# Kernel tuning notes

Hardware: AMD Instinct MI355X
Metric: run time of the kernel (lower is better)

Reference implementation:

```python
import math
import jax, jax.numpy as jnp
import numpy as np

HID = 2048      # hidden_size
NH = 16         # num_heads
KD = HID // NH  # key head dim = 128 (even, required by XPOS)
VD = HID        # value_dim (value_factor=1)
VHD = VD // NH  # value head dim
SCALE_BASE = 512
ROPE_BASE = 10000.0
GN_EPS = 1e-5


def _rotate_every_two(x):
    x1 = x[..., ::2]
    x2 = x[..., 1::2]
    return jnp.stack((-x2, x1), axis=-1).reshape(x.shape)


def _dup(a):  # repeat_interleave(x, 2, dim=-1)
    return jnp.repeat(a, 2, axis=-1)


def _xpos_apply(x, pos, inv_freq, xpos_scale, downscale):
    # x: [B, H, S, KD], pos: [B, S]
    posf = pos.astype(jnp.float32)
    angles = posf[:, :, None] * inv_freq[None, None, :]          # [B, S, KD/2]
    sin = _dup(jnp.sin(angles))[:, None]                          # [B, 1, S, KD]
    cos = _dup(jnp.cos(angles))[:, None]
    scale = xpos_scale[None, None, :] ** (posf[:, :, None] / SCALE_BASE)
    if downscale:
        scale = 1.0 / scale
    scale = _dup(scale)[:, None]                                  # [B, 1, S, KD]
    return (x * cos + _rotate_every_two(x) * sin) * scale


def setup_inputs() -> dict:
    key = jax.random.key(0)
    ks = jax.random.split(key, 6)
    B, S = 1, 2048
    std = 1.0 / HID
    x = jax.random.normal(ks[0], (B, S, HID), dtype=jnp.float32)
    position_ids = jnp.broadcast_to(jnp.arange(S, dtype=jnp.int64), (B, S))
    Wq = jax.random.normal(ks[1], (HID, HID), dtype=jnp.float32) * std
    Wk = jax.random.normal(ks[2], (HID, HID), dtype=jnp.float32) * std
    Wv = jax.random.normal(ks[3], (HID, VD), dtype=jnp.float32) * std
    Wg = jax.random.normal(ks[4], (HID, VD), dtype=jnp.float32) * std
    Wo = jax.random.normal(ks[5], (VD, HID), dtype=jnp.float32) * std
    gn_weight = jnp.ones((VD,), dtype=jnp.float32)
    gn_bias = jnp.zeros((VD,), dtype=jnp.float32)
    return {"x": x, "position_ids": position_ids, "Wq": Wq, "Wk": Wk,
            "Wv": Wv, "Wg": Wg, "Wo": Wo,
            "gn_weight": gn_weight, "gn_bias": gn_bias}


def reference(x, position_ids, Wq, Wk, Wv, Wg, Wo, gn_weight, gn_bias):
    B, S, _ = x.shape
    # XPOS / multiscale-decay buffers (deterministic, as in XPOSRelativePosition)
    inv_freq = 1.0 / (ROPE_BASE ** (jnp.arange(0, KD, 2, dtype=jnp.float32) / KD))
    xpos_scale = (jnp.arange(0, KD, 2, dtype=jnp.float32) + 0.4 * KD) / (1.4 * KD)
    gamma = 1.0 - jnp.exp(jnp.linspace(math.log(1.0 / 32), math.log(1.0 / 512), NH))
    log_gamma = jnp.log(gamma)                                    # [NH]

    # projections -> [B, H, S, d]
    q = (x @ Wq).reshape(B, S, NH, KD).transpose(0, 2, 1, 3)
    k = (x @ Wk).reshape(B, S, NH, KD).transpose(0, 2, 1, 3)
    v = (x @ Wv).reshape(B, S, NH, VHD).transpose(0, 2, 1, 3)
    g = x @ Wg                                                    # [B, S, VD]

    q = _xpos_apply(q, position_ids, inv_freq, xpos_scale, downscale=False)
    k = _xpos_apply(k, position_ids, inv_freq, xpos_scale, downscale=True)

    # decay mask: exp(log_gamma * (i-j)) for i>=j else 0   [B, H, S, S]
    relpos = position_ids[:, :, None] - position_ids[:, None, :]  # [B, S, S]
    decay = jnp.exp(log_gamma[None, :, None, None]
                    * jnp.maximum(relpos, 0)[:, None].astype(jnp.float32))
    decay = decay * (relpos >= 0)[:, None].astype(jnp.float32)

    scores = jnp.einsum('bhqd,bhkd->bhqk', q, k) * decay          # [B, H, S, S]
    retained = jnp.einsum('bhqk,bhkv->bhqv', scores, v)           # [B, H, S, VHD]

    # GroupNorm(num_heads, value_dim): normalize each head group per token
    r = retained.transpose(0, 2, 1, 3)                            # [B, S, H, VHD]
    mean = r.mean(axis=-1, keepdims=True)
    var = r.var(axis=-1, keepdims=True)
    rn = (r - mean) * jax.lax.rsqrt(var + GN_EPS)
    rn = rn * gn_weight.reshape(NH, VHD) + gn_bias.reshape(NH, VHD)
    rn = rn.reshape(B, S, VD)

    out = (jax.nn.silu(g) * rn) @ Wo                              # [B, S, HID]
    return out
```

## Files before the change

kernel.cpp:

```cpp
#include <hip/hip_runtime.h>
#include <math.h>

#define S_LEN 2048
#define HIDD  2048
#define NHEAD 16
#define HD    128

#define TILE_SH 4096

typedef __attribute__((ext_vector_type(8))) short short8;
typedef __attribute__((ext_vector_type(4))) float float4v;
typedef unsigned short ushort_t;

static __device__ __forceinline__ ushort_t f2bf(float f) {
    unsigned int u = __float_as_uint(f);
    u += 0x7fff + ((u >> 16) & 1);
    return (ushort_t)(u >> 16);
}
static __device__ __forceinline__ float bf2f(ushort_t s) {
    return __uint_as_float(((unsigned int)s) << 16);
}
__device__ __forceinline__ float silu_f(float x) { return x / (1.f + expf(-x)); }

__device__ __forceinline__ void gl_lds16(const ushort_t* g, short* l) {
    __builtin_amdgcn_global_load_lds((const __attribute__((address_space(1))) void*)g,
                                     (__attribute__((address_space(3))) void*)l, 16, 0, 0);
}

__global__ __launch_bounds__(256)
void split_kernel(const float* __restrict__ in, ushort_t* __restrict__ hi,
                  ushort_t* __restrict__ lo, int n4)
{
    const int i = blockIdx.x * 256 + threadIdx.x;
    if (i >= n4) return;
    const float4 v = ((const float4*)in)[i];
    ushort4 h, l;
    h.x = f2bf(v.x); l.x = f2bf(v.x - bf2f(h.x));
    h.y = f2bf(v.y); l.y = f2bf(v.y - bf2f(h.y));
    h.z = f2bf(v.z); l.z = f2bf(v.z - bf2f(h.z));
    h.w = f2bf(v.w); l.w = f2bf(v.w - bf2f(h.w));
    const int row = i >> 9, c4 = (i & 511) * 4;
    const size_t off = ((size_t)((row >> 7) * 64 + (c4 >> 5))) * TILE_SH
                     + (row & 127) * 32 + (c4 & 31);
    *(ushort4*)&hi[off] = h;
    *(ushort4*)&lo[off] = l;
}

__global__ __launch_bounds__(256)
void addp_kernel(float* __restrict__ out, const float* __restrict__ p, int n4)
{
    const int i = blockIdx.x * 256 + threadIdx.x;
    if (i >= n4) return;
    float4 a = ((const float4*)out)[i];
    const float4 b = ((const float4*)p)[i];
    a.x += b.x; a.y += b.y; a.z += b.z; a.w += b.w;
    ((float4*)out)[i] = a;
}

__global__ __launch_bounds__(256)
void split_transpose_all(const float* __restrict__ W0, const float* __restrict__ W1,
                         const float* __restrict__ W2, const float* __restrict__ W3,
                         const float* __restrict__ W4, ushort_t* __restrict__ wt)
{
    __shared__ float t[64][65];
    const size_t PL = (size_t)HIDD * HIDD;
    const int z = blockIdx.z;
    const float* W = (z == 0) ? W0 : (z == 1) ? W1 : (z == 2) ? W2 : (z == 3) ? W3 : W4;
    ushort_t* Thi = wt + (size_t)z * 2 * PL;
    ushort_t* Tlo = Thi + PL;

    const int k0 = blockIdx.y * 64, n0 = blockIdx.x * 64;
    const int tx = threadIdx.x & 15, ty = threadIdx.x >> 4;
    #pragma unroll
    for (int it = 0; it < 4; it++) {
        const int k = ty + it * 16;
        const float4 v = *(const float4*)&W[(size_t)(k0 + k) * HIDD + n0 + tx * 4];
        t[k][tx * 4 + 0] = v.x; t[k][tx * 4 + 1] = v.y;
        t[k][tx * 4 + 2] = v.z; t[k][tx * 4 + 3] = v.w;
    }
    __syncthreads();
    #pragma unroll
    for (int it = 0; it < 4; it++) {
        const int n = ty + it * 16;
        ushort4 h, l; float a;
        a = t[tx * 4 + 0][n]; h.x = f2bf(a); l.x = f2bf(a - bf2f(h.x));
        a = t[tx * 4 + 1][n]; h.y = f2bf(a); l.y = f2bf(a - bf2f(h.y));
        a = t[tx * 4 + 2][n]; h.z = f2bf(a); l.z = f2bf(a - bf2f(h.z));
        a = t[tx * 4 + 3][n]; h.w = f2bf(a); l.w = f2bf(a - bf2f(h.w));
        const int nn_ = n0 + n, kk_ = k0 + tx * 4;
        const size_t off = ((size_t)((nn_ >> 7) * 64 + (kk_ >> 5))) * TILE_SH
                         + (nn_ & 127) * 32 + (kk_ & 31);
        *(ushort4*)&Thi[off] = h;
        *(ushort4*)&Tlo[off] = l;
    }
}

template<int MODE>
__global__ __launch_bounds__(256, 2)
void mfma_gemm(const ushort_t* __restrict__ Ahi, const ushort_t* __restrict__ Alo,
               const ushort_t* __restrict__ WT, const int* __restrict__ pos_ids,
               ushort_t* __restrict__ qhi, ushort_t* __restrict__ qlo,
               ushort_t* __restrict__ khi, ushort_t* __restrict__ klo,
               ushort_t* __restrict__ vThi, ushort_t* __restrict__ vTlo,
               float* __restrict__ gbuf, float* __restrict__ outC, int mbase)
{
    __shared__ __align__(16) short sm[(MODE == 1) ? 16896 : 8448];

    const int tid = threadIdx.x;
    const int w = tid >> 6, L = tid & 63;
    const int qd = L >> 4, lc = L & 15;
    const int lin = blockIdx.x;
    int n0, m0, kh = 0;
    if (MODE == 0) {
        n0 = (((lin & 7) << 3) + ((lin >> 3) & 7)) << 7;
        m0 = mbase + ((lin >> 6) << 7);
    } else {
        n0 = (lin & 15) << 7;
        m0 = ((lin >> 4) & 15) << 7;
        kh = lin >> 8;
    }
    const size_t PL = (size_t)HIDD * HIDD;

    int sel, nn;
    const ushort_t *Bhi, *Blo;
    if (MODE == 0) {
        sel = n0 >> 11; nn = n0 & 2047;
        Bhi = WT + (size_t)sel * 2 * PL; Blo = Bhi + PL;
    } else {
        sel = -1; nn = n0;
        Bhi = WT; Blo = WT + PL;
    }

    const int sdoff = (w >> 1) * 4096 + (w & 1) * 2048 + L * 8;
    const ushort_t* sbase = ((w < 2) ? Bhi : Blo) + (size_t)(nn >> 7) * 64 * TILE_SH
                          + (w & 1) * 2048 + L * 8;

    const ushort_t* aTh = Ahi + (size_t)(m0 >> 7) * 64 * TILE_SH;
    const ushort_t* aTl = Alo + (size_t)(m0 >> 7) * 64 * TILE_SH;

    const int wm = (w & 1) * 64, wn = (w >> 1) * 64;
    int aoff[4], boff[4];
    #pragma unroll
    for (int i = 0; i < 4; i++) aoff[i] = (wm + i * 16 + lc) * 32 + qd * 8;
    #pragma unroll
    for (int j = 0; j < 4; j++) boff[j] = (wn + j * 16 + lc) * 32 + qd * 8;

    float4v acc[4][4];
    #pragma unroll
    for (int i = 0; i < 4; i++)
        #pragma unroll
        for (int j = 0; j < 4; j++)
            #pragma unroll
            for (int r = 0; r < 4; r++) acc[i][j][r] = 0.f;

    const int kt0 = (MODE == 1) ? kh * 32 : 0;
    const int kt1 = (MODE == 1) ? kt0 + 32 : 64;

    if (MODE == 0) {
        for (int kt = kt0; kt < kt1; kt++) {
            const size_t ko = (size_t)kt * TILE_SH;
            short8 ahf[4], alf[4];
            #pragma unroll
            for (int i = 0; i < 4; i++) {
                ahf[i] = *(const short8*)(aTh + ko + aoff[i]);
                alf[i] = *(const short8*)(aTl + ko + aoff[i]);
            }
            #pragma unroll
            for (int t = 0; t < 4; t++)
                gl_lds16(sbase + ko + t * 512, sm + sdoff + t * 512);
            __syncthreads();

            short8 bhf[4], blf[4];
            #pragma unroll
            for (int j = 0; j < 4; j++) {
                bhf[j] = *(const short8*)(sm + boff[j]);
                blf[j] = *(const short8*)(sm + 4096 + boff[j]);
            }
            #pragma unroll
            for (int i = 0; i < 4; i++)
                #pragma unroll
                for (int j = 0; j < 4; j++) {
                    acc[i][j] = __builtin_amdgcn_mfma_f32_16x16x32_bf16(ahf[i], bhf[j], acc[i][j], 0, 0, 0);
                    acc[i][j] = __builtin_amdgcn_mfma_f32_16x16x32_bf16(alf[i], bhf[j], acc[i][j], 0, 0, 0);
                    acc[i][j] = __builtin_amdgcn_mfma_f32_16x16x32_bf16(ahf[i], blf[j], acc[i][j], 0, 0, 0);
                }
            __syncthreads();
        }
    } else {
        #pragma unroll
        for (int t = 0; t < 4; t++)
            gl_lds16(sbase + (size_t)kt0 * TILE_SH + t * 512, sm + sdoff + t * 512);
        asm volatile("s_waitcnt vmcnt(0)" ::: "memory");
        __builtin_amdgcn_s_barrier();
        __builtin_amdgcn_sched_barrier(0);

        int cur = 0;
        for (int kt = kt0; kt < kt1; kt++) {
            if (kt + 1 < kt1) {
                const size_t kn = (size_t)(kt + 1) * TILE_SH;
                short* nb = sm + (cur ^ 1) * 8192;
                #pragma unroll
                for (int t = 0; t < 4; t++)
                    gl_lds16(sbase + kn + t * 512, nb + sdoff + t * 512);
            }
            const size_t ko = (size_t)kt * TILE_SH;
            short8 ahf[4], alf[4];
            #pragma unroll
            for (int i = 0; i < 4; i++) {
                ahf[i] = *(const short8*)(aTh + ko + aoff[i]);
                alf[i] = *(const short8*)(aTl + ko + aoff[i]);
            }
            const short* cb = sm + cur * 8192;
            short8 bhf[4], blf[4];
            #pragma unroll
            for (int j = 0; j < 4; j++) {
                bhf[j] = *(const short8*)(cb + boff[j]);
                blf[j] = *(const short8*)(cb + 4096 + boff[j]);
            }
            #pragma unroll
            for (int i = 0; i < 4; i++)
                #pragma unroll
                for (int j = 0; j < 4; j++) {
                    acc[i][j] = __builtin_amdgcn_mfma_f32_16x16x32_bf16(ahf[i], bhf[j], acc[i][j], 0, 0, 0);
                    acc[i][j] = __builtin_amdgcn_mfma_f32_16x16x32_bf16(alf[i], bhf[j], acc[i][j], 0, 0, 0);
                    acc[i][j] = __builtin_amdgcn_mfma_f32_16x16x32_bf16(ahf[i], blf[j], acc[i][j], 0, 0, 0);
                }
            asm volatile("s_waitcnt vmcnt(0)" ::: "memory");
            __builtin_amdgcn_s_barrier();
            __builtin_amdgcn_sched_barrier(0);
            cur ^= 1;
        }
    }

    float* ob = (float*)sm;
    const int half = w & 1;
    const int head = nn >> 7;

    #pragma unroll
    for (int i = 0; i < 4; i++) {
        #pragma unroll
        for (int j = 0; j < 4; j++)
            #pragma unroll
            for (int r = 0; r < 4; r++)
                ob[(half * 16 + qd * 4 + r) * 132 + wn + j * 16 + lc] = acc[i][j][r];
        __syncthreads();

        if (MODE == 1 || sel == 3) {
            float* dst = (MODE == 1) ? (kh ? gbuf : outC) : gbuf;
            #pragma unroll
            for (int p = 0; p < 4; p++) {
                const int row = p * 8 + (tid >> 5);
                const int c = (tid & 31) * 4;
                const int grow = m0 + (row >> 4) * 64 + i * 16 + (row & 15);
                const float4 vv = *(const float4*)&ob[row * 132 + c];
                *(float4*)&dst[(size_t)grow * HIDD + nn + c] = vv;
            }
        } else if (sel == 2) {
            const int d = tid >> 1, hs = tid & 1;
            const int sbase2 = m0 + hs * 64 + i * 16;
            short8 h0, h1, l0, l1;
            #pragma unroll
            for (int sp = 0; sp < 8; sp++) {
                float a = ob[(hs * 16 + sp) * 132 + d];
                ushort_t hb = f2bf(a);
                h0[sp] = (short)hb; l0[sp] = (short)f2bf(a - bf2f(hb));
                a = ob[(hs * 16 + 8 + sp) * 132 + d];
                hb = f2bf(a);
                h1[sp] = (short)hb; l1[sp] = (short)f2bf(a - bf2f(hb));
            }
            ushort_t* dh = vThi + ((size_t)head * HD + d) * S_LEN + sbase2;
            ushort_t* dl = vTlo + ((size_t)head * HD + d) * S_LEN + sbase2;
            *(short8*)dh = h0; *(short8*)(dh + 8) = h1;
            *(short8*)dl = l0; *(short8*)(dl + 8) = l1;
        } else {
            const float sgn = (sel == 0) ? 1.f : -1.f;
            ushort_t* dhb = (sel == 0) ? qhi : khi;
            ushort_t* dlb = (sel == 0) ? qlo : klo;
            #pragma unroll
            for (int p = 0; p < 2; p++) {
                const int row = p * 16 + (tid >> 4);
                const int c8 = (tid & 15) * 8;
                const int grow = m0 + (row >> 4) * 64 + i * 16 + (row & 15);
                const float pos = (float)pos_ids[grow];
                const float pe = sgn * pos * (1.f / 512.f);
                short8 hv, lv;
                #pragma unroll
                for (int pp = 0; pp < 4; pp++) {
                    const int d = c8 + pp * 2;
                    const float v0 = ob[row * 132 + d], v1 = ob[row * 132 + d + 1];
                    const float invf = exp2f(-(float)d * (13.28771238f / 128.f));
                    float s, c_; sincosf(pos * invf, &s, &c_);
                    const float scl = exp2f(log2f(((float)d + 51.2f) * (1.f / 179.2f)) * pe);
                    const float e0 = (v0 * c_ - v1 * s) * scl;
                    const float e1 = (v1 * c_ + v0 * s) * scl;
                    const ushort_t h0 = f2bf(e0), h1 = f2bf(e1);
                    hv[pp * 2] = (short)h0;  hv[pp * 2 + 1] = (short)h1;
                    lv[pp * 2] = (short)f2bf(e0 - bf2f(h0));
                    lv[pp * 2 + 1] = (short)f2bf(e1 - bf2f(h1));
                }
                *(short8*)&dhb[((size_t)head * S_LEN + grow) * HD + c8] = hv;
                *(short8*)&dlb[((size_t)head * S_LEN + grow) * HD + c8] = lv;
            }
        }
        __syncthreads();
    }
}

#define KROW 136
#define VROW 40
#define KH_  0
#define KL_  (32 * KROW)
#define VH_  (2 * 32 * KROW)
#define VL_  (VH_ + 128 * VROW)
#define PH_  (VH_ + 2 * 128 * VROW)
#define PLO_ (PH_ + 64 * VROW)
#define YH_  8704
#define YL_  (YH_ + 64 * KROW)
__global__ __launch_bounds__(256, 2)
void retention2(const ushort_t* __restrict__ qhi, const ushort_t* __restrict__ qlo,
                const ushort_t* __restrict__ khi, const ushort_t* __restrict__ klo,
                const ushort_t* __restrict__ vThi, const ushort_t* __restrict__ vTlo,
                const float* __restrict__ gbuf, const float* __restrict__ gnw,
                const float* __restrict__ gnb,
                ushort_t* __restrict__ yhi, ushort_t* __restrict__ ylo)
{
    __shared__ __align__(16) short sm[26112];

    const int h = blockIdx.y;
    const int qb = (gridDim.x - 1) - blockIdx.x;
    const int r0 = qb * 64;
    const int tid = threadIdx.x;
    const int w = tid >> 6, L = tid & 63;
    const int qd = L >> 4, lc = L & 15;

    const float e = -3.4657359f + (float)h * ((-6.2383246f + 3.4657359f) / 15.f);
    const float lg2g = logf(1.f - expf(e)) * 1.44269504f;

    short8 qfh[4], qfl[4];
    {
        const size_t qb0 = ((size_t)h * S_LEN + r0 + w * 16 + lc) * HD + qd * 8;
        #pragma unroll
        for (int ks = 0; ks < 4; ks++) {
            qfh[ks] = *(const short8*)(qhi + qb0 + ks * 32);
            qfl[ks] = *(const short8*)(qlo + qb0 + ks * 32);
        }
    }

    float4v osum[2][4];
    #pragma unroll
    for (int mt = 0; mt < 2; mt++)
        #pragma unroll
        for (int j = 0; j < 4; j++)
            #pragma unroll
            for (int r = 0; r < 4; r++) osum[mt][j][r] = 0.f;

    const int qh_ = w >> 1, vh_ = w & 1;
    const int nch = (r0 + 64) / 32;

    for (int ch = 0; ch < nch; ch++) {
        const int kg0 = ch * 32;
        #pragma unroll
        for (int t = 0; t < 4; t++) {
            const int c = t * 256 + tid;
            const int p = c >> 9, r = (c >> 4) & 31, qq = c & 15;
            const ushort_t* src = (p ? klo : khi) + ((size_t)h * S_LEN + kg0 + r) * HD + qq * 8;
            *(short8*)(sm + (p ? KL_ : KH_) + r * KROW + qq * 8) = *(const short8*)src;
        }
        #pragma unroll
        for (int t = 0; t < 4; t++) {
            const int c = t * 256 + tid;
            const int p = c >> 9, r = (c >> 2) & 127, qq = c & 3;
            const ushort_t* src = (p ? vTlo : vThi) + ((size_t)h * HD + r) * S_LEN + kg0 + qq * 8;
            *(short8*)(sm + (p ? VL_ : VH_) + r * VROW + qq * 8) = *(const short8*)src;
        }
        __syncthreads();

        float4v sacc[2];
        #pragma unroll
        for (int j = 0; j < 2; j++)
            #pragma unroll
            for (int r = 0; r < 4; r++) sacc[j][r] = 0.f;
        #pragma unroll
        for (int ks = 0; ks < 4; ks++) {
            #pragma unroll
            for (int j = 0; j < 2; j++) {
                const short8 bh = *(const short8*)(sm + KH_ + (j * 16 + lc) * KROW + ks * 32 + qd * 8);
                const short8 bl = *(const short8*)(sm + KL_ + (j * 16 + lc) * KROW + ks * 32 + qd * 8);
                sacc[j] = __builtin_amdgcn_mfma_f32_16x16x32_bf16(qfh[ks], bh, sacc[j], 0, 0, 0);
                sacc[j] = __builtin_amdgcn_mfma_f32_16x16x32_bf16(qfl[ks], bh, sacc[j], 0, 0, 0);
                sacc[j] = __builtin_amdgcn_mfma_f32_16x16x32_bf16(qfh[ks], bl, sacc[j], 0, 0, 0);
            }
        }
        #pragma unroll
        for (int j = 0; j < 2; j++)
            #pragma unroll
            for (int r = 0; r < 4; r++) {
                const int dq = (r0 + w * 16 + qd * 4 + r) - (kg0 + j * 16 + lc);
                const float p = (dq >= 0) ? sacc[j][r] * exp2f(lg2g * (float)dq) : 0.f;
                const ushort_t hb = f2bf(p);
                const int off = (w * 16 + qd * 4 + r) * VROW + j * 16 + lc;
                sm[PH_ + off]  = (short)hb;
                sm[PLO_ + off] = (short)f2bf(p - bf2f(hb));
            }
        __syncthreads();

        #pragma unroll
        for (int mt = 0; mt < 2; mt++) {
            const short8 pfh = *(const short8*)(sm + PH_  + (qh_ * 32 + mt * 16 + lc) * VROW + qd * 8);
            const short8 pfl = *(const short8*)(sm + PLO_ + (qh_ * 32 + mt * 16 + lc) * VROW + qd * 8);
            #pragma unroll
            for (int j = 0; j < 4; j++) {
                const short8 vfh = *(const short8*)(sm + VH_ + (vh_ * 64 + j * 16 + lc) * VROW + qd * 8);
                const short8 vfl = *(const short8*)(sm + VL_ + (vh_ * 64 + j * 16 + lc) * VROW + qd * 8);
                osum[mt][j] = __builtin_amdgcn_mfma_f32_16x16x32_bf16(pfh, vfh, osum[mt][j], 0, 0, 0);
                osum[mt][j] = __builtin_amdgcn_mfma_f32_16x16x32_bf16(pfl, vfh, osum[mt][j], 0, 0, 0);
                osum[mt][j] = __builtin_amdgcn_mfma_f32_16x16x32_bf16(pfh, vfl, osum[mt][j], 0, 0, 0);
            }
        }
        __syncthreads();
    }

    float* fr = (float*)sm;
    #pragma unroll
    for (int mt = 0; mt < 2; mt++)
        #pragma unroll
        for (int r = 0; r < 4; r++) {
            float s1 = 0.f, s2 = 0.f;
            #pragma unroll
            for (int j = 0; j < 4; j++) { const float v = osum[mt][j][r]; s1 += v; s2 += v * v; }
            const int row = qh_ * 32 + mt * 16 + qd * 4 + r;
            fr[row * 32 + vh_ * 16 + lc] = s1;
            fr[2048 + row * 32 + vh_ * 16 + lc] = s2;
        }
    __syncthreads();
    if (tid < 64) {
        float s1 = 0.f, s2 = 0.f;
        #pragma unroll
        for (int t = 0; t < 32; t++) { s1 += fr[tid * 32 + t]; s2 += fr[2048 + tid * 32 + t]; }
        const float mean = s1 * (1.f / 128.f);
        const float var  = s2 * (1.f / 128.f) - mean * mean;
        fr[4096 + tid] = mean;
        fr[4160 + tid] = 1.f / sqrtf(var + 1e-5f);
    }
    __syncthreads();

    #pragma unroll
    for (int mt = 0; mt < 2; mt++)
        #pragma unroll
        for (int r = 0; r < 4; r++) {
            const int row = qh_ * 32 + mt * 16 + qd * 4 + r;
            const float mean = fr[4096 + row], inv = fr[4160 + row];
            const int grow = r0 + row;
            #pragma unroll
            for (int j = 0; j < 4; j++) {
                const int col = vh_ * 64 + j * 16 + lc;
                const float gv = gbuf[(size_t)grow * HIDD + h * HD + col];
                const float o = ((osum[mt][j][r] - mean) * inv * gnw[h * HD + col]
                                 + gnb[h * HD + col]) * silu_f(gv);
                const ushort_t hb = f2bf(o);
                sm[YH_ + row * KROW + col] = (short)hb;
                sm[YL_ + row * KROW + col] = (short)f2bf(o - bf2f(hb));
            }
        }
    __syncthreads();
    {
        const int r_ = tid >> 2, cs = (tid & 3) * 32;
        const int grow = r0 + r_;
        const size_t tb = ((size_t)((grow >> 7) * 64 + h * 4 + (tid & 3))) * TILE_SH
                        + (grow & 127) * 32;
        #pragma unroll
        for (int c8 = 0; c8 < 4; c8++) {
            *(short8*)(yhi + tb + c8 * 8) = *(const short8*)(sm + YH_ + r_ * KROW + cs + c8 * 8);
            *(short8*)(ylo + tb + c8 * 8) = *(const short8*)(sm + YL_ + r_ * KROW + cs + c8 * 8);
        }
    }
}

extern "C" void kernel_launch(void* const* d_in, const int* in_sizes, int n_in,
                              void* d_out, int out_size, void* d_ws, size_t ws_size,
                              hipStream_t stream) {
    const float* x   = (const float*)d_in[0];
    const int*   pid = (const int*)d_in[1];
    const float* gnw = (const float*)d_in[7];
    const float* gnb = (const float*)d_in[8];
    float* out = (float*)d_out;
    (void)in_sizes; (void)n_in; (void)out_size; (void)ws_size;

    const size_t PL = (size_t)HIDD * HIDD;

    ushort_t* wt   = (ushort_t*)d_ws;
    ushort_t* xhi  = wt + 10 * PL;
    ushort_t* xlo  = xhi + PL;
    ushort_t* qhi_ = xlo + PL;
    ushort_t* qlo_ = qhi_ + PL;
    ushort_t* khi_ = qlo_ + PL;
    ushort_t* klo_ = khi_ + PL;
    ushort_t* vThi = klo_ + PL;
    ushort_t* vTlo = vThi + PL;
    float*    gbuf = (float*)(vTlo + PL);
    ushort_t* yhi  = (ushort_t*)(gbuf + PL);
    ushort_t* ylo  = yhi + PL;
    float*    p1   = (float*)xhi;

    split_kernel<<<(int)(PL / 4 / 256), 256, 0, stream>>>(x, xhi, xlo, (int)(PL / 4));
    split_transpose_all<<<dim3(32, 32, 5), 256, 0, stream>>>(
        (const float*)d_in[2], (const float*)d_in[3], (const float*)d_in[4],
        (const float*)d_in[5], (const float*)d_in[6], wt);

    mfma_gemm<0><<<512, 256, 0, stream>>>(xhi, xlo, wt, pid,
        qhi_, qlo_, khi_, klo_, vThi, vTlo, gbuf, nullptr, 0);
    mfma_gemm<0><<<512, 256, 0, stream>>>(xhi, xlo, wt, pid,
        qhi_, qlo_, khi_, klo_, vThi, vTlo, gbuf, nullptr, 1024);

    retention2<<<dim3(32, 16), 256, 0, stream>>>(qhi_, qlo_, khi_, klo_, vThi, vTlo,
        gbuf, gnw, gnb, yhi, ylo);

    mfma_gemm<1><<<512, 256, 0, stream>>>(yhi, ylo, wt + 8 * PL, pid,
        nullptr, nullptr, nullptr, nullptr, nullptr, nullptr, p1, out, 0);

    addp_kernel<<<(int)(PL / 4 / 256), 256, 0, stream>>>(out, p1, (int)(PL / 4));
}
```

Before: 553.1 us.

## Split long causal retention query blocks across two workgroups and add separate GroupNorm epilogue

```diff
diff --git a/kernel.cpp b/kernel.cpp
--- a/kernel.cpp
+++ b/kernel.cpp
@@ -314,20 +314,27 @@
 #define VL_  (VH_ + 128 * VROW)
 #define PH_  (VH_ + 2 * 128 * VROW)
 #define PLO_ (PH_ + 64 * VROW)
-#define YH_  8704
-#define YL_  (YH_ + 64 * KROW)
-__global__ __launch_bounds__(256, 2)
+__global__ __launch_bounds__(256, 3)
 void retention2(const ushort_t* __restrict__ qhi, const ushort_t* __restrict__ qlo,
                 const ushort_t* __restrict__ khi, const ushort_t* __restrict__ klo,
                 const ushort_t* __restrict__ vThi, const ushort_t* __restrict__ vTlo,
-                const float* __restrict__ gbuf, const float* __restrict__ gnw,
-                const float* __restrict__ gnb,
-                ushort_t* __restrict__ yhi, ushort_t* __restrict__ ylo)
+                float* __restrict__ posum)
 {
-    __shared__ __align__(16) short sm[26112];
-
-    const int h = blockIdx.y;
-    const int qb = (gridDim.x - 1) - blockIdx.x;
+    __shared__ __align__(16) short sm[24064];
+
+    const int bx = blockIdx.x;
+    const int h = bx & 15;
+    const int u = bx >> 4;
+    const int g = u / 3, r3 = u % 3;
+    int qb, c0, c1, part;
+    if (r3 < 2) {
+        qb = 31 - g; part = r3;
+        const int hchunks = qb + 1;
+        c0 = r3 * hchunks; c1 = c0 + hchunks;
+    } else {
+        qb = 15 - g; part = 0;
+        c0 = 0; c1 = 2 * (qb + 1);
+    }
     const int r0 = qb * 64;
     const int tid = threadIdx.x;
     const int w = tid >> 6, L = tid & 63;
@@ -355,9 +362,8 @@
             for (int r = 0; r < 4; r++) osum[mt][j][r] = 0.f;
 
     const int qh_ = w >> 1, vh_ = w & 1;
-    const int nch = (r0 + 64) / 32;
-
-    for (int ch = 0; ch < nch; ch++) {
+
+    for (int ch = c0; ch < c1; ch++) {
         const int kg0 = ch * 32;
         #pragma unroll
         for (int t = 0; t < 4; t++) {
@@ -420,59 +426,72 @@
         __syncthreads();
     }
 
-    float* fr = (float*)sm;
+    float* pdst = posum + (((size_t)(h * 32 + qb) * 2 + part) * 8192);
     #pragma unroll
     for (int mt = 0; mt < 2; mt++)
         #pragma unroll
-        for (int r = 0; r < 4; r++) {
-            float s1 = 0.f, s2 = 0.f;
-            #pragma unroll
-            for (int j = 0; j < 4; j++) { const float v = osum[mt][j][r]; s1 += v; s2 += v * v; }
-            const int row = qh_ * 32 + mt * 16 + qd * 4 + r;
-            fr[row * 32 + vh_ * 16 + lc] = s1;
-            fr[2048 + row * 32 + vh_ * 16 + lc] = s2;
-        }
+        for (int j = 0; j < 4; j++)
+            #pragma unroll
+            for (int r = 0; r < 4; r++) {
+                const int row = qh_ * 32 + mt * 16 + qd * 4 + r;
+                const int col = vh_ * 64 + j * 16 + lc;
+                pdst[row * 128 + col] = osum[mt][j][r];
+            }
+}
+
+#define EKROW 136
+__global__ __launch_bounds__(256, 2)
+void gn_epilogue(const float* __restrict__ posum, const float* __restrict__ gbuf,
+                 const float* __restrict__ gnw, const float* __restrict__ gnb,
+                 ushort_t* __restrict__ yhi, ushort_t* __restrict__ ylo)
+{
+    __shared__ __align__(16) short sm[2 * 64 * EKROW];
+    const int qb = blockIdx.x, h = blockIdx.y;
+    const int tid = threadIdx.x;
+    const int row = tid >> 2;
+    const int cq = (tid & 3) * 32;
+    const int grow = qb * 64 + row;
+    const float* p0 = posum + ((size_t)(h * 32 + qb) * 2) * 8192 + row * 128;
+    const float* p1 = p0 + 8192;
+    const bool two = (qb >= 16);
+
+    float v[32];
+    float s1 = 0.f, s2 = 0.f;
+    #pragma unroll
+    for (int c = 0; c < 32; c += 4) {
+        float4 a = *(const float4*)&p0[cq + c];
+        if (two) {
+            const float4 b = *(const float4*)&p1[cq + c];
+            a.x += b.x; a.y += b.y; a.z += b.z; a.w += b.w;
+        }
+        v[c] = a.x; v[c + 1] = a.y; v[c + 2] = a.z; v[c + 3] = a.w;
+        s1 += a.x + a.y + a.z + a.w;
+        s2 += a.x * a.x + a.y * a.y + a.z * a.z + a.w * a.w;
+    }
+    s1 += __shfl_xor(s1, 1); s2 += __shfl_xor(s2, 1);
+    s1 += __shfl_xor(s1, 2); s2 += __shfl_xor(s2, 2);
+    const float mean = s1 * (1.f / 128.f);
+    const float inv = 1.f / sqrtf(s2 * (1.f / 128.f) - mean * mean + 1e-5f);
+
+    #pragma unroll
+    for (int c = 0; c < 32; c++) {
+        const int col = cq + c;
+        const float gv = gbuf[(size_t)grow * HIDD + h * HD + col];
+        const float o = ((v[c] - mean) * inv * gnw[h * HD + col] + gnb[h * HD + col])
+                      * silu_f(gv);
+        const ushort_t hb = f2bf(o);
+        sm[row * EKROW + col] = (short)hb;
+        sm[64 * EKROW + row * EKROW + col] = (short)f2bf(o - bf2f(hb));
+    }
     __syncthreads();
-    if (tid < 64) {
-        float s1 = 0.f, s2 = 0.f;
-        #pragma unroll
-        for (int t = 0; t < 32; t++) { s1 += fr[tid * 32 + t]; s2 += fr[2048 + tid * 32 + t]; }
-        const float mean = s1 * (1.f / 128.f);
-        const float var  = s2 * (1.f / 128.f) - mean * mean;
-        fr[4096 + tid] = mean;
-        fr[4160 + tid] = 1.f / sqrtf(var + 1e-5f);
-    }
-    __syncthreads();
-
-    #pragma unroll
-    for (int mt = 0; mt < 2; mt++)
-        #pragma unroll
-        for (int r = 0; r < 4; r++) {
-            const int row = qh_ * 32 + mt * 16 + qd * 4 + r;
-            const float mean = fr[4096 + row], inv = fr[4160 + row];
-            const int grow = r0 + row;
-            #pragma unroll
-            for (int j = 0; j < 4; j++) {
-                const int col = vh_ * 64 + j * 16 + lc;
-                const float gv = gbuf[(size_t)grow * HIDD + h * HD + col];
-                const float o = ((osum[mt][j][r] - mean) * inv * gnw[h * HD + col]
-                                 + gnb[h * HD + col]) * silu_f(gv);
-                const ushort_t hb = f2bf(o);
-                sm[YH_ + row * KROW + col] = (short)hb;
-                sm[YL_ + row * KROW + col] = (short)f2bf(o - bf2f(hb));
-            }
-        }
-    __syncthreads();
-    {
-        const int r_ = tid >> 2, cs = (tid & 3) * 32;
-        const int grow = r0 + r_;
-        const size_t tb = ((size_t)((grow >> 7) * 64 + h * 4 + (tid & 3))) * TILE_SH
-                        + (grow & 127) * 32;
-        #pragma unroll
-        for (int c8 = 0; c8 < 4; c8++) {
-            *(short8*)(yhi + tb + c8 * 8) = *(const short8*)(sm + YH_ + r_ * KROW + cs + c8 * 8);
-            *(short8*)(ylo + tb + c8 * 8) = *(const short8*)(sm + YL_ + r_ * KROW + cs + c8 * 8);
-        }
+    const int r_ = tid >> 2, cs = (tid & 3) * 32;
+    const int g2 = qb * 64 + r_;
+    const size_t tb = ((size_t)((g2 >> 7) * 64 + h * 4 + (tid & 3))) * TILE_SH
+                    + (g2 & 127) * 32;
+    #pragma unroll
+    for (int c8 = 0; c8 < 4; c8++) {
+        *(short8*)(yhi + tb + c8 * 8) = *(const short8*)(sm + r_ * EKROW + cs + c8 * 8);
+        *(short8*)(ylo + tb + c8 * 8) = *(const short8*)(sm + 64 * EKROW + r_ * EKROW + cs + c8 * 8);
     }
 }
 
@@ -501,6 +520,7 @@
     ushort_t* yhi  = (ushort_t*)(gbuf + PL);
     ushort_t* ylo  = yhi + PL;
     float*    p1   = (float*)xhi;
+    float*    posum = (float*)wt;
 
     split_kernel<<<(int)(PL / 4 / 256), 256, 0, stream>>>(x, xhi, xlo, (int)(PL / 4));
     split_transpose_all<<<dim3(32, 32, 5), 256, 0, stream>>>(
@@ -512,8 +532,9 @@
     mfma_gemm<0><<<512, 256, 0, stream>>>(xhi, xlo, wt, pid,
         qhi_, qlo_, khi_, klo_, vThi, vTlo, gbuf, nullptr, 1024);
 
-    retention2<<<dim3(32, 16), 256, 0, stream>>>(qhi_, qlo_, khi_, klo_, vThi, vTlo,
-        gbuf, gnw, gnb, yhi, ylo);
+    retention2<<<768, 256, 0, stream>>>(qhi_, qlo_, khi_, klo_, vThi, vTlo, posum);
+
+    gn_epilogue<<<dim3(32, 16), 256, 0, stream>>>(posum, gbuf, gnw, gnb, yhi, ylo);
 
     mfma_gemm<1><<<512, 256, 0, stream>>>(yhi, ylo, wt + 8 * PL, pid,
         nullptr, nullptr, nullptr, nullptr, nullptr, nullptr, p1, out, 0);
```

New measurement: 508.4 us. 8.1% less time.
